# Performance work log

Measured on AMD Instinct MI355X. Metric: run time of the kernel, lower is better.

## Reference

```python
import jax, jax.numpy as jnp
import numpy as np

N, E, IN_FT, OUT_FT = 20000, 4096, 128, 128


def setup_inputs() -> dict:
    key = jax.random.key(0)
    kx, kh, kw = jax.random.split(key, 3)
    X = jax.random.normal(kx, (N, IN_FT), dtype=jnp.float32)
    H = jax.random.randint(kh, (N, E), 0, 2, dtype=jnp.int32)
    weight = jax.random.normal(kw, (IN_FT, OUT_FT), dtype=jnp.float32) * (1.0 / np.sqrt(IN_FT))
    bias = jnp.zeros((OUT_FT,), dtype=jnp.float32)
    return {"X": X, "H": H, "weight": weight, "bias": bias}


def reference(X, H, weight, bias):
    # Dv^{-1/2} H De^{-1} H^T Dv^{-1/2} X W + b, with diag matrices fused as
    # row/column scalings (same math as the torch.diag @ chain, no NxN temporaries).
    Hf = H.astype(jnp.float32)
    v_deg = jnp.sum(Hf, axis=1)            # [N]
    e_deg = jnp.sum(Hf, axis=0)            # [E]
    v_deg = jnp.where(v_deg > 0, v_deg, 1.0)
    e_deg = jnp.where(e_deg > 0, e_deg, 1.0)
    dv_inv_sqrt = 1.0 / jnp.sqrt(v_deg)    # diag(Dv^-1/2)
    de_inv = 1.0 / e_deg                   # diag(De^-1)
    Y = dv_inv_sqrt[:, None] * X
    T = Hf.T @ Y                           # H^T (...)        [E, in]
    T = de_inv[:, None] * T                # De^-1 (...)
    Z = Hf @ T                             # H (...)          [N, in]
    Z = dv_inv_sqrt[:, None] * Z           # Dv^-1/2 (...)
    out = Z @ weight + bias                # [N, out]
    return out
```

## Files before the change

### kernel.cpp

```cpp
#include <hip/hip_runtime.h>

#define NV 20000
#define NE 4096
#define FT 128
#define NW_E 128
#define NW_V 625
#define PT_STRIDE 632
#define NKC 313

typedef __attribute__((ext_vector_type(8))) short short8v;
typedef __attribute__((ext_vector_type(4))) float float4v;

__device__ __forceinline__ unsigned short f2bf(float f) {
    unsigned u = __float_as_uint(f);
    u += 0x7FFFu + ((u >> 16) & 1u);
    return (unsigned short)(u >> 16);
}
__device__ __forceinline__ int lds_off(int r, int chunk) {
    return r * 128 + ((chunk ^ (r & 7)) << 4);
}
__device__ __forceinline__ uint4 lut_entry(int t) {
    uint4 e;
    e.x = ((t & 1) ? 0x3F80u : 0u) | ((t & 2) ? 0x3F800000u : 0u);
    e.y = ((t & 4) ? 0x3F80u : 0u) | ((t & 8) ? 0x3F800000u : 0u);
    e.z = ((t & 16) ? 0x3F80u : 0u) | ((t & 32) ? 0x3F800000u : 0u);
    e.w = ((t & 64) ? 0x3F80u : 0u) | ((t & 128) ? 0x3F800000u : 0u);
    return e;
}

__global__ __launch_bounds__(256) void k_pack(const int* __restrict__ H,
                                              unsigned* __restrict__ packed,
                                              float* __restrict__ dv) {
    __shared__ int cl[4];
    int t = threadIdx.x, wave = t >> 6, lane = t & 63;
    int row = blockIdx.x * 2 + (wave >> 1);
    int half = wave & 1;
    const uint4* base = reinterpret_cast<const uint4*>(H) + (size_t)row * 1024 + half * 512 + lane * 8;
    unsigned m = 0;
#pragma unroll
    for (int i = 0; i < 8; ++i) {
        uint4 v = base[i];
        m |= (v.x ? 1u : 0u) << (i * 4 + 0);
        m |= (v.y ? 1u : 0u) << (i * 4 + 1);
        m |= (v.z ? 1u : 0u) << (i * 4 + 2);
        m |= (v.w ? 1u : 0u) << (i * 4 + 3);
    }
    packed[(size_t)row * NW_E + half * 64 + lane] = m;
    int c = __popc(m);
    for (int o = 32; o > 0; o >>= 1) c += __shfl_down(c, o, 64);
    if (lane == 0) cl[wave] = c;
    __syncthreads();
    if (t < 2) {
        int d = cl[t * 2] + cl[t * 2 + 1];
        dv[blockIdx.x * 2 + t] = d > 0 ? 1.0f / sqrtf((float)d) : 1.0f;
    }
}

__global__ __launch_bounds__(256) void k_btrans(const unsigned* __restrict__ packed,
                                                unsigned* __restrict__ packedT) {
    int lane = threadIdx.x & 63;
    int w = threadIdx.x >> 6;
    int ew = blockIdx.y * 4 + w;
    int n = blockIdx.x * 64 + lane;
    unsigned wv = (n < NV) ? packed[(size_t)n * NW_E + ew] : 0u;
    unsigned my = 0;
#pragma unroll
    for (int j = 0; j < 32; ++j) {
        unsigned long long m = __ballot(((wv >> j) & 1u) != 0);
        unsigned part = (lane < 32) ? (unsigned)m : (unsigned)(m >> 32);
        if ((lane & 31) == j) my = part;
    }
    int nw = blockIdx.x * 2 + (lane >> 5);
    int e = ew * 32 + (lane & 31);
    if (nw <= 625) packedT[(size_t)e * PT_STRIDE + nw] = my;
}

__global__ __launch_bounds__(256) void k_mid(const unsigned* __restrict__ packedT,
                                             const float* __restrict__ X,
                                             const float* __restrict__ dv,
                                             float* __restrict__ de,
                                             unsigned short* __restrict__ At) {
    int b = blockIdx.x, t = threadIdx.x;
    int wave = t >> 6, lane = t & 63;
    if (b < 1024) {
        int e = b * 4 + wave;
        const unsigned* row = packedT + (size_t)e * PT_STRIDE;
        int c = 0;
        for (int i = lane; i < NW_V; i += 64) c += __popc(row[i]);
        for (int o = 32; o > 0; o >>= 1) c += __shfl_down(c, o, 64);
        if (lane == 0) de[e] = c > 0 ? 1.0f / (float)c : 1.0f;
    } else if (b < 2274) {
        int b2 = b - 1024;
        int f = t & 127;
        int nb = (b2 * 2 + (t >> 7)) * 8;
        unsigned short h[8];
#pragma unroll
        for (int i = 0; i < 8; ++i) {
            int n = nb + i;
            h[i] = f2bf(X[(size_t)n * FT + f] * dv[n]);
        }
        uint4 u;
        u.x = (unsigned)h[0] | ((unsigned)h[1] << 16);
        u.y = (unsigned)h[2] | ((unsigned)h[3] << 16);
        u.z = (unsigned)h[4] | ((unsigned)h[5] << 16);
        u.w = (unsigned)h[6] | ((unsigned)h[7] << 16);
        int kc = nb >> 6;
        *reinterpret_cast<uint4*>(At + (size_t)kc * 8192 + f * 64 + (nb & 63)) = u;
    } else {
        int f = t & 127;
        uint4 z = {0, 0, 0, 0};
        *reinterpret_cast<uint4*>(At + (size_t)312 * 8192 + f * 64 + 32 + (t >> 7) * 8) = z;
        *reinterpret_cast<uint4*>(At + (size_t)312 * 8192 + f * 64 + 48 + (t >> 7) * 8) = z;
    }
}

__global__ __launch_bounds__(256, 2) void k_mm1(const unsigned short* __restrict__ At,
                                                const unsigned* __restrict__ packedT,
                                                float* __restrict__ P, int chunkK) {
    __shared__ __align__(16) unsigned char sA[16384];
    __shared__ __align__(16) unsigned char sB[16384];
    __shared__ __align__(16) uint4 slut[256];
    int t = threadIdx.x;
    slut[t] = lut_entry(t);

    int et = blockIdx.x & 31, kp = blockIdx.x >> 5;
    int e0 = et * 128;
    int kbeg = kp * chunkK;
    int kend = kbeg + chunkK; if (kend > NKC * 64) kend = NKC * 64;
    int iters = (kend - kbeg) >> 6; if (iters < 0) iters = 0;

    float4v acc[4][4];
#pragma unroll
    for (int i = 0; i < 4; ++i)
#pragma unroll
        for (int j = 0; j < 4; ++j)
#pragma unroll
            for (int r = 0; r < 4; ++r) acc[i][j][r] = 0.0f;

    int wave = t >> 6, lane = t & 63;
    int wm0 = (wave & 1) * 64, wc0 = (wave >> 1) * 64;
    int r0 = lane & 15, q = lane >> 4;

    const unsigned* brow = packedT + (size_t)(e0 + (t & 127)) * PT_STRIDE + (kbeg >> 5);
    uint4 bw, bw2;
    if (t < 128) bw = *reinterpret_cast<const uint4*>(brow);
    __syncthreads();

    for (int it = 0; it < iters; ++it) {
        int kc = (kbeg >> 6) + it;
        const uint4* slab = reinterpret_cast<const uint4*>(At + (size_t)kc * 8192);
#pragma unroll
        for (int c = 0; c < 4; ++c) {
            int idx = c * 256 + t;
            uint4 v = slab[idx];
            *reinterpret_cast<uint4*>(sA + lds_off(idx >> 3, idx & 7)) = v;
        }
        if (t < 128) {
            unsigned w0, w1;
            if (!(it & 1)) {
                bw2 = *reinterpret_cast<const uint4*>(brow + 2 * it + 4);
                w0 = bw.x; w1 = bw.y;
            } else {
                w0 = bw.z; w1 = bw.w;
            }
            int rB = t;
#pragma unroll
            for (int c = 0; c < 4; ++c)
                *reinterpret_cast<uint4*>(sB + lds_off(rB, c)) = slut[(w0 >> (c * 8)) & 0xFF];
#pragma unroll
            for (int c = 0; c < 4; ++c)
                *reinterpret_cast<uint4*>(sB + lds_off(rB, 4 + c)) = slut[(w1 >> (c * 8)) & 0xFF];
            if (it & 1) bw = bw2;
        }
        __syncthreads();
#pragma unroll
        for (int ks = 0; ks < 2; ++ks) {
            short8v a[4], bb[4];
#pragma unroll
            for (int mi = 0; mi < 4; ++mi)
                a[mi] = *reinterpret_cast<const short8v*>(sA + lds_off(wm0 + mi * 16 + r0, ks * 4 + q));
#pragma unroll
            for (int ci = 0; ci < 4; ++ci)
                bb[ci] = *reinterpret_cast<const short8v*>(sB + lds_off(wc0 + ci * 16 + r0, ks * 4 + q));
#pragma unroll
            for (int mi = 0; mi < 4; ++mi)
#pragma unroll
                for (int ci = 0; ci < 4; ++ci)
                    acc[mi][ci] = __builtin_amdgcn_mfma_f32_16x16x32_bf16(a[mi], bb[ci], acc[mi][ci], 0, 0, 0);
        }
        __syncthreads();
    }
    float* Pp = P + (size_t)kp * (128 * 4096);
#pragma unroll
    for (int mi = 0; mi < 4; ++mi)
#pragma unroll
        for (int ci = 0; ci < 4; ++ci) {
            int f = wm0 + mi * 16 + q * 4;
            int e = e0 + wc0 + ci * 16 + r0;
#pragma unroll
            for (int r = 0; r < 4; ++r)
                Pp[(size_t)(f + r) * 4096 + e] = acc[mi][ci][r];
        }
}

__global__ __launch_bounds__(256) void k_reduce(const float4v* __restrict__ P,
                                                float4v* __restrict__ Tt, int S) {
    int i = blockIdx.x * 256 + threadIdx.x;
    float4v a = P[i];
    for (int p = 1; p < S; ++p) a += P[(size_t)p * 131072 + i];
    Tt[i] = a;
}

__global__ __launch_bounds__(256) void k_ut(const float* __restrict__ Tt,
                                            const float* __restrict__ W,
                                            const float* __restrict__ de,
                                            unsigned short* __restrict__ Ut) {
    int t = threadIdx.x;
    int bx = blockIdx.x;
    int e = bx * 64 + (t & 63);
    int g0 = blockIdx.y * 16 + (t >> 6) * 4;
    float a0 = 0, a1 = 0, a2 = 0, a3 = 0;
    for (int f = 0; f < 128; ++f) {
        float tv = Tt[(size_t)f * 4096 + e];
        float4 wv = *reinterpret_cast<const float4*>(W + f * 128 + g0);
        a0 += tv * wv.x; a1 += tv * wv.y; a2 += tv * wv.z; a3 += tv * wv.w;
    }
    float d = de[e];
    int j = t & 63;
    Ut[(size_t)bx * 8192 + (g0 + 0) * 64 + j] = f2bf(a0 * d);
    Ut[(size_t)bx * 8192 + (g0 + 1) * 64 + j] = f2bf(a1 * d);
    Ut[(size_t)bx * 8192 + (g0 + 2) * 64 + j] = f2bf(a2 * d);
    Ut[(size_t)bx * 8192 + (g0 + 3) * 64 + j] = f2bf(a3 * d);
}

__global__ __launch_bounds__(256, 4) void k_mm2(const unsigned* __restrict__ packed,
                                                const unsigned short* __restrict__ Ut,
                                                const float* __restrict__ dv,
                                                const float* __restrict__ bias,
                                                float* __restrict__ out) {
    __shared__ __align__(16) unsigned char sA[16384];
    __shared__ __align__(16) unsigned char sB[4096];
    __shared__ __align__(16) uint4 slut[256];
    int t = threadIdx.x;
    slut[t] = lut_entry(t);

    int mt = blockIdx.x >> 2, qg = blockIdx.x & 3;
    int n0 = mt * 128, g0 = qg * 32;

    float4v acc[4];
#pragma unroll
    for (int i = 0; i < 4; ++i)
#pragma unroll
        for (int r = 0; r < 4; ++r) acc[i][r] = 0.0f;

    int wave = t >> 6, lane = t & 63;
    int wm0 = (wave & 1) * 64, wc0 = (wave >> 1) * 16;
    int r0 = lane & 15, q = lane >> 4;

    const unsigned* arow = packed + (size_t)(n0 + (t & 127)) * NW_E;
    const unsigned short* bbase = Ut + (size_t)qg * 2048;
    int t2 = t - 128;
    uint4 aw, aw2;
    if (t < 128) aw = *reinterpret_cast<const uint4*>(arow);
    __syncthreads();

    for (int it = 0; it < 64; ++it) {
        if (t < 128) {
            unsigned w0, w1;
            if (!(it & 1)) {
                aw2 = *reinterpret_cast<const uint4*>(arow + 2 * it + 4);
                w0 = aw.x; w1 = aw.y;
            } else {
                w0 = aw.z; w1 = aw.w;
            }
            int rA = t;
#pragma unroll
            for (int c = 0; c < 4; ++c)
                *reinterpret_cast<uint4*>(sA + lds_off(rA, c)) = slut[(w0 >> (c * 8)) & 0xFF];
#pragma unroll
            for (int c = 0; c < 4; ++c)
                *reinterpret_cast<uint4*>(sA + lds_off(rA, 4 + c)) = slut[(w1 >> (c * 8)) & 0xFF];
            if (it & 1) aw = aw2;
        } else {
            const uint4* src = reinterpret_cast<const uint4*>(bbase + (size_t)it * 8192);
#pragma unroll
            for (int c = 0; c < 2; ++c) {
                int idx = t2 * 2 + c;
                uint4 v = src[idx];
                *reinterpret_cast<uint4*>(sB + lds_off(idx >> 3, idx & 7)) = v;
            }
        }
        __syncthreads();
#pragma unroll
        for (int ks = 0; ks < 2; ++ks) {
            short8v a[4], bb;
#pragma unroll
            for (int mi = 0; mi < 4; ++mi)
                a[mi] = *reinterpret_cast<const short8v*>(sA + lds_off(wm0 + mi * 16 + r0, ks * 4 + q));
            bb = *reinterpret_cast<const short8v*>(sB + lds_off(wc0 + r0, ks * 4 + q));
#pragma unroll
            for (int mi = 0; mi < 4; ++mi)
                acc[mi] = __builtin_amdgcn_mfma_f32_16x16x32_bf16(a[mi], bb, acc[mi], 0, 0, 0);
        }
        __syncthreads();
    }
    {
        int g = g0 + wc0 + r0;
        float bg = bias[g];
#pragma unroll
        for (int mi = 0; mi < 4; ++mi) {
#pragma unroll
            for (int r = 0; r < 4; ++r) {
                int n = n0 + wm0 + mi * 16 + q * 4 + r;
                if (n < NV) out[(size_t)n * 128 + g] = dv[n] * acc[mi][r] + bg;
            }
        }
    }
}

extern "C" void kernel_launch(void* const* d_in, const int* in_sizes, int n_in,
                              void* d_out, int out_size, void* d_ws, size_t ws_size,
                              hipStream_t stream) {
    const float* X    = (const float*)d_in[0];
    const int*   H    = (const int*)d_in[1];
    const float* W    = (const float*)d_in[2];
    const float* bias = (const float*)d_in[3];
    float* out = (float*)d_out;

    char* ws = (char*)d_ws;
    size_t off = 0;
    auto alloc = [&](size_t sz) { char* p = ws + off; off += (sz + 255) & ~(size_t)255; return p; };
    unsigned*       packed  = (unsigned*)alloc((size_t)NV * NW_E * 4);
    unsigned*       packedT = (unsigned*)alloc((size_t)NE * PT_STRIDE * 4);
    unsigned short* At      = (unsigned short*)alloc((size_t)NKC * 8192 * 2);
    float*          Tt      = (float*)alloc((size_t)FT * NE * 4);
    unsigned short* Ut      = (unsigned short*)alloc((size_t)FT * NE * 2);
    float*          dv      = (float*)alloc((size_t)NV * 4);
    float*          de      = (float*)alloc((size_t)NE * 4);
    size_t fixed = off;

    long long avail = (long long)ws_size - (long long)fixed;
    int S = (int)(avail / (128LL * 4096 * 4));
    if (S > 16) S = 16;
    if (S < 1) S = 1;
    float* P1 = (float*)(ws + fixed);
    int chunkK = ((NKC * 64 + S * 64 - 1) / (S * 64)) * 64;

    k_pack  <<<NV / 2, 256, 0, stream>>>(H, packed, dv);
    k_btrans<<<dim3(313, 32), 256, 0, stream>>>(packed, packedT);
    k_mid   <<<2275, 256, 0, stream>>>(packedT, X, dv, de, At);
    k_mm1   <<<32 * S, 256, 0, stream>>>(At, packedT, P1, chunkK);
    k_reduce<<<512, 256, 0, stream>>>((const float4v*)P1, (float4v*)Tt, S);
    k_ut    <<<dim3(64, 8), 256, 0, stream>>>(Tt, W, de, Ut);
    k_mm2   <<<628, 256, 0, stream>>>(packed, Ut, dv, bias, out);
}
```

Measured before the change: 592.8 us.

## Double K-tile depth, use direct global-to-LDS loads, fold edge-degree count into transpose

Both bf16 MFMA GEMM kernels now process 128-wide K slabs instead of 64, so the per-iteration barrier and bit-unpack overhead is amortized over twice the MFMA work. The A and B operand tiles are pre-swizzled in global memory so they can be copied straight into LDS with global_load_lds, skipping the register round trip. The edge-degree reduction moves out of k_mid into atomics inside the bit-transpose kernel, removing a separate pass over packedT. LDS usage doubles, which may lower occupancy. k_mm2 launch bounds drop to 3 blocks per SM.

```diff
diff --git a/kernel.cpp b/kernel.cpp
--- a/kernel.cpp
+++ b/kernel.cpp
@@ -6,7 +6,8 @@
 #define NW_E 128
 #define NW_V 625
 #define PT_STRIDE 632
-#define NKC 313
+#define NKC2 157
+#define K_TOT 20096
 
 typedef __attribute__((ext_vector_type(8))) short short8v;
 typedef __attribute__((ext_vector_type(4))) float float4v;
@@ -16,8 +17,8 @@
     u += 0x7FFFu + ((u >> 16) & 1u);
     return (unsigned short)(u >> 16);
 }
-__device__ __forceinline__ int lds_off(int r, int chunk) {
-    return r * 128 + ((chunk ^ (r & 7)) << 4);
+__device__ __forceinline__ int lds_off(int r, int c) {
+    return r * 256 + ((c ^ (r & 15)) << 4);
 }
 __device__ __forceinline__ uint4 lut_entry(int t) {
     uint4 e;
@@ -27,12 +28,18 @@
     e.w = ((t & 64) ? 0x3F80u : 0u) | ((t & 128) ? 0x3F800000u : 0u);
     return e;
 }
+__device__ __forceinline__ void cp16(void* l, const void* g) {
+    __builtin_amdgcn_global_load_lds((__attribute__((address_space(1))) void*)g,
+                                     (__attribute__((address_space(3))) void*)l, 16, 0, 0);
+}
 
 __global__ __launch_bounds__(256) void k_pack(const int* __restrict__ H,
                                               unsigned* __restrict__ packed,
-                                              float* __restrict__ dv) {
+                                              float* __restrict__ dv,
+                                              int* __restrict__ de_cnt) {
     __shared__ int cl[4];
     int t = threadIdx.x, wave = t >> 6, lane = t & 63;
+    if (blockIdx.x < 16) de_cnt[blockIdx.x * 256 + t] = 0;
     int row = blockIdx.x * 2 + (wave >> 1);
     int half = wave & 1;
     const uint4* base = reinterpret_cast<const uint4*>(H) + (size_t)row * 1024 + half * 512 + lane * 8;
@@ -57,7 +64,8 @@
 }
 
 __global__ __launch_bounds__(256) void k_btrans(const unsigned* __restrict__ packed,
-                                                unsigned* __restrict__ packedT) {
+                                                unsigned* __restrict__ packedT,
+                                                int* __restrict__ de_cnt) {
     int lane = threadIdx.x & 63;
     int w = threadIdx.x >> 6;
     int ew = blockIdx.y * 4 + w;
@@ -73,52 +81,40 @@
     int nw = blockIdx.x * 2 + (lane >> 5);
     int e = ew * 32 + (lane & 31);
     if (nw <= 625) packedT[(size_t)e * PT_STRIDE + nw] = my;
-}
-
-__global__ __launch_bounds__(256) void k_mid(const unsigned* __restrict__ packedT,
-                                             const float* __restrict__ X,
+    int cnt = __popc(my);
+    cnt += __shfl_down(cnt, 32, 64);
+    if (lane < 32) atomicAdd(de_cnt + e, cnt);
+}
+
+__global__ __launch_bounds__(256) void k_mid(const float* __restrict__ X,
                                              const float* __restrict__ dv,
-                                             float* __restrict__ de,
                                              unsigned short* __restrict__ At) {
-    int b = blockIdx.x, t = threadIdx.x;
-    int wave = t >> 6, lane = t & 63;
-    if (b < 1024) {
-        int e = b * 4 + wave;
-        const unsigned* row = packedT + (size_t)e * PT_STRIDE;
-        int c = 0;
-        for (int i = lane; i < NW_V; i += 64) c += __popc(row[i]);
-        for (int o = 32; o > 0; o >>= 1) c += __shfl_down(c, o, 64);
-        if (lane == 0) de[e] = c > 0 ? 1.0f / (float)c : 1.0f;
-    } else if (b < 2274) {
-        int b2 = b - 1024;
-        int f = t & 127;
-        int nb = (b2 * 2 + (t >> 7)) * 8;
-        unsigned short h[8];
-#pragma unroll
-        for (int i = 0; i < 8; ++i) {
-            int n = nb + i;
-            h[i] = f2bf(X[(size_t)n * FT + f] * dv[n]);
-        }
-        uint4 u;
-        u.x = (unsigned)h[0] | ((unsigned)h[1] << 16);
-        u.y = (unsigned)h[2] | ((unsigned)h[3] << 16);
-        u.z = (unsigned)h[4] | ((unsigned)h[5] << 16);
-        u.w = (unsigned)h[6] | ((unsigned)h[7] << 16);
-        int kc = nb >> 6;
-        *reinterpret_cast<uint4*>(At + (size_t)kc * 8192 + f * 64 + (nb & 63)) = u;
-    } else {
-        int f = t & 127;
-        uint4 z = {0, 0, 0, 0};
-        *reinterpret_cast<uint4*>(At + (size_t)312 * 8192 + f * 64 + 32 + (t >> 7) * 8) = z;
-        *reinterpret_cast<uint4*>(At + (size_t)312 * 8192 + f * 64 + 48 + (t >> 7) * 8) = z;
-    }
+    int t = threadIdx.x;
+    int f = t & 127;
+    int item = blockIdx.x * 2 + (t >> 7);
+    int nbase = item * 8;
+    unsigned short h[8];
+#pragma unroll
+    for (int i = 0; i < 8; ++i) {
+        int n = nbase + i;
+        float v = (n < NV) ? X[(size_t)n * FT + f] * dv[n] : 0.0f;
+        h[i] = f2bf(v);
+    }
+    uint4 u;
+    u.x = (unsigned)h[0] | ((unsigned)h[1] << 16);
+    u.y = (unsigned)h[2] | ((unsigned)h[3] << 16);
+    u.z = (unsigned)h[4] | ((unsigned)h[5] << 16);
+    u.w = (unsigned)h[6] | ((unsigned)h[7] << 16);
+    int kc2 = nbase >> 7;
+    int c = (nbase >> 3) & 15;
+    *reinterpret_cast<uint4*>(At + (size_t)kc2 * 16384 + f * 128 + ((c ^ (f & 15)) << 3)) = u;
 }
 
 __global__ __launch_bounds__(256, 2) void k_mm1(const unsigned short* __restrict__ At,
                                                 const unsigned* __restrict__ packedT,
                                                 float* __restrict__ P, int chunkK) {
-    __shared__ __align__(16) unsigned char sA[16384];
-    __shared__ __align__(16) unsigned char sB[16384];
+    __shared__ __align__(16) unsigned char sA[32768];
+    __shared__ __align__(16) unsigned char sB[32768];
     __shared__ __align__(16) uint4 slut[256];
     int t = threadIdx.x;
     slut[t] = lut_entry(t);
@@ -126,8 +122,8 @@
     int et = blockIdx.x & 31, kp = blockIdx.x >> 5;
     int e0 = et * 128;
     int kbeg = kp * chunkK;
-    int kend = kbeg + chunkK; if (kend > NKC * 64) kend = NKC * 64;
-    int iters = (kend - kbeg) >> 6; if (iters < 0) iters = 0;
+    int kend = kbeg + chunkK; if (kend > K_TOT) kend = K_TOT;
+    int iters = (kend - kbeg) >> 7; if (iters < 0) iters = 0;
 
     float4v acc[4][4];
 #pragma unroll
@@ -141,40 +137,30 @@
     int wm0 = (wave & 1) * 64, wc0 = (wave >> 1) * 64;
     int r0 = lane & 15, q = lane >> 4;
 
-    const unsigned* brow = packedT + (size_t)(e0 + (t & 127)) * PT_STRIDE + (kbeg >> 5);
-    uint4 bw, bw2;
-    if (t < 128) bw = *reinterpret_cast<const uint4*>(brow);
+    const uint4* brow4 = reinterpret_cast<const uint4*>(
+        packedT + (size_t)(e0 + (t & 127)) * PT_STRIDE + (kbeg >> 5));
+    uint4 bw;
+    if (t < 128 && iters > 0) bw = *brow4;
     __syncthreads();
 
+    const char* gA = reinterpret_cast<const char*>(At) + (size_t)(kbeg >> 7) * 32768 + wave * 8192 + lane * 16;
+    char* lA = reinterpret_cast<char*>(sA) + wave * 8192;
+
     for (int it = 0; it < iters; ++it) {
-        int kc = (kbeg >> 6) + it;
-        const uint4* slab = reinterpret_cast<const uint4*>(At + (size_t)kc * 8192);
-#pragma unroll
-        for (int c = 0; c < 4; ++c) {
-            int idx = c * 256 + t;
-            uint4 v = slab[idx];
-            *reinterpret_cast<uint4*>(sA + lds_off(idx >> 3, idx & 7)) = v;
-        }
+        const char* g = gA + (size_t)it * 32768;
+#pragma unroll
+        for (int j = 0; j < 8; ++j) cp16(lA + j * 1024, g + j * 1024);
         if (t < 128) {
-            unsigned w0, w1;
-            if (!(it & 1)) {
-                bw2 = *reinterpret_cast<const uint4*>(brow + 2 * it + 4);
-                w0 = bw.x; w1 = bw.y;
-            } else {
-                w0 = bw.z; w1 = bw.w;
-            }
-            int rB = t;
-#pragma unroll
-            for (int c = 0; c < 4; ++c)
-                *reinterpret_cast<uint4*>(sB + lds_off(rB, c)) = slut[(w0 >> (c * 8)) & 0xFF];
-#pragma unroll
-            for (int c = 0; c < 4; ++c)
-                *reinterpret_cast<uint4*>(sB + lds_off(rB, 4 + c)) = slut[(w1 >> (c * 8)) & 0xFF];
-            if (it & 1) bw = bw2;
+            uint4 nxt = brow4[it + 1];
+            unsigned wd[4] = {bw.x, bw.y, bw.z, bw.w};
+#pragma unroll
+            for (int c = 0; c < 16; ++c)
+                *reinterpret_cast<uint4*>(sB + lds_off(t, c)) = slut[(wd[c >> 2] >> ((c & 3) * 8)) & 0xFF];
+            bw = nxt;
         }
         __syncthreads();
 #pragma unroll
-        for (int ks = 0; ks < 2; ++ks) {
+        for (int ks = 0; ks < 4; ++ks) {
             short8v a[4], bb[4];
 #pragma unroll
             for (int mi = 0; mi < 4; ++mi)
@@ -213,11 +199,12 @@
 
 __global__ __launch_bounds__(256) void k_ut(const float* __restrict__ Tt,
                                             const float* __restrict__ W,
-                                            const float* __restrict__ de,
+                                            const int* __restrict__ de_cnt,
                                             unsigned short* __restrict__ Ut) {
     int t = threadIdx.x;
     int bx = blockIdx.x;
-    int e = bx * 64 + (t & 63);
+    int j = t & 63;
+    int e = bx * 64 + j;
     int g0 = blockIdx.y * 16 + (t >> 6) * 4;
     float a0 = 0, a1 = 0, a2 = 0, a3 = 0;
     for (int f = 0; f < 128; ++f) {
@@ -225,21 +212,27 @@
         float4 wv = *reinterpret_cast<const float4*>(W + f * 128 + g0);
         a0 += tv * wv.x; a1 += tv * wv.y; a2 += tv * wv.z; a3 += tv * wv.w;
     }
-    float d = de[e];
-    int j = t & 63;
-    Ut[(size_t)bx * 8192 + (g0 + 0) * 64 + j] = f2bf(a0 * d);
-    Ut[(size_t)bx * 8192 + (g0 + 1) * 64 + j] = f2bf(a1 * d);
-    Ut[(size_t)bx * 8192 + (g0 + 2) * 64 + j] = f2bf(a2 * d);
-    Ut[(size_t)bx * 8192 + (g0 + 3) * 64 + j] = f2bf(a3 * d);
-}
-
-__global__ __launch_bounds__(256, 4) void k_mm2(const unsigned* __restrict__ packed,
+    int cnt = de_cnt[e];
+    float d = cnt > 0 ? 1.0f / (float)cnt : 1.0f;
+    float av[4] = {a0, a1, a2, a3};
+    int slabB = bx >> 1;
+    int chi = ((bx & 1) << 3) | (j >> 3);
+    int pos = j & 7;
+#pragma unroll
+    for (int k = 0; k < 4; ++k) {
+        int g = g0 + k;
+        int qg = g >> 5, gr = g & 31;
+        Ut[(size_t)(qg * 32 + slabB) * 4096 + gr * 128 + ((chi ^ (gr & 15)) << 3) + pos] = f2bf(av[k] * d);
+    }
+}
+
+__global__ __launch_bounds__(256, 3) void k_mm2(const unsigned* __restrict__ packed,
                                                 const unsigned short* __restrict__ Ut,
                                                 const float* __restrict__ dv,
                                                 const float* __restrict__ bias,
                                                 float* __restrict__ out) {
-    __shared__ __align__(16) unsigned char sA[16384];
-    __shared__ __align__(16) unsigned char sB[4096];
+    __shared__ __align__(16) unsigned char sA[32768];
+    __shared__ __align__(16) unsigned char sB[8192];
     __shared__ __align__(16) uint4 slut[256];
     int t = threadIdx.x;
     slut[t] = lut_entry(t);
@@ -257,42 +250,31 @@
     int wm0 = (wave & 1) * 64, wc0 = (wave >> 1) * 16;
     int r0 = lane & 15, q = lane >> 4;
 
-    const unsigned* arow = packed + (size_t)(n0 + (t & 127)) * NW_E;
-    const unsigned short* bbase = Ut + (size_t)qg * 2048;
-    int t2 = t - 128;
-    uint4 aw, aw2;
-    if (t < 128) aw = *reinterpret_cast<const uint4*>(arow);
+    const uint4* arow4 = reinterpret_cast<const uint4*>(packed + (size_t)(n0 + (t & 127)) * NW_E);
+    uint4 aw;
+    if (t < 128) aw = *arow4;
     __syncthreads();
 
-    for (int it = 0; it < 64; ++it) {
+    int wb = wave & 1;
+    const char* gB = reinterpret_cast<const char*>(Ut) + (size_t)(qg * 32) * 8192 + wb * 4096 + lane * 16;
+    char* lB = reinterpret_cast<char*>(sB) + wb * 4096;
+
+    for (int it = 0; it < 32; ++it) {
         if (t < 128) {
-            unsigned w0, w1;
-            if (!(it & 1)) {
-                aw2 = *reinterpret_cast<const uint4*>(arow + 2 * it + 4);
-                w0 = aw.x; w1 = aw.y;
-            } else {
-                w0 = aw.z; w1 = aw.w;
-            }
-            int rA = t;
-#pragma unroll
-            for (int c = 0; c < 4; ++c)
-                *reinterpret_cast<uint4*>(sA + lds_off(rA, c)) = slut[(w0 >> (c * 8)) & 0xFF];
-#pragma unroll
-            for (int c = 0; c < 4; ++c)
-                *reinterpret_cast<uint4*>(sA + lds_off(rA, 4 + c)) = slut[(w1 >> (c * 8)) & 0xFF];
-            if (it & 1) aw = aw2;
+            uint4 nxt = arow4[it + 1];
+            unsigned wd[4] = {aw.x, aw.y, aw.z, aw.w};
+#pragma unroll
+            for (int c = 0; c < 16; ++c)
+                *reinterpret_cast<uint4*>(sA + lds_off(t, c)) = slut[(wd[c >> 2] >> ((c & 3) * 8)) & 0xFF];
+            aw = nxt;
         } else {
-            const uint4* src = reinterpret_cast<const uint4*>(bbase + (size_t)it * 8192);
-#pragma unroll
-            for (int c = 0; c < 2; ++c) {
-                int idx = t2 * 2 + c;
-                uint4 v = src[idx];
-                *reinterpret_cast<uint4*>(sB + lds_off(idx >> 3, idx & 7)) = v;
-            }
+            const char* g = gB + (size_t)it * 8192;
+#pragma unroll
+            for (int j = 0; j < 4; ++j) cp16(lB + j * 1024, g + j * 1024);
         }
         __syncthreads();
 #pragma unroll
-        for (int ks = 0; ks < 2; ++ks) {
+        for (int ks = 0; ks < 4; ++ks) {
             short8v a[4], bb;
 #pragma unroll
             for (int mi = 0; mi < 4; ++mi)
@@ -332,11 +314,11 @@
     auto alloc = [&](size_t sz) { char* p = ws + off; off += (sz + 255) & ~(size_t)255; return p; };
     unsigned*       packed  = (unsigned*)alloc((size_t)NV * NW_E * 4);
     unsigned*       packedT = (unsigned*)alloc((size_t)NE * PT_STRIDE * 4);
-    unsigned short* At      = (unsigned short*)alloc((size_t)NKC * 8192 * 2);
+    unsigned short* At      = (unsigned short*)alloc((size_t)NKC2 * 16384 * 2);
     float*          Tt      = (float*)alloc((size_t)FT * NE * 4);
     unsigned short* Ut      = (unsigned short*)alloc((size_t)FT * NE * 2);
     float*          dv      = (float*)alloc((size_t)NV * 4);
-    float*          de      = (float*)alloc((size_t)NE * 4);
+    int*            de_cnt  = (int*)alloc((size_t)NE * 4);
     size_t fixed = off;
 
     long long avail = (long long)ws_size - (long long)fixed;
@@ -344,13 +326,13 @@
     if (S > 16) S = 16;
     if (S < 1) S = 1;
     float* P1 = (float*)(ws + fixed);
-    int chunkK = ((NKC * 64 + S * 64 - 1) / (S * 64)) * 64;
-
-    k_pack  <<<NV / 2, 256, 0, stream>>>(H, packed, dv);
-    k_btrans<<<dim3(313, 32), 256, 0, stream>>>(packed, packedT);
-    k_mid   <<<2275, 256, 0, stream>>>(packedT, X, dv, de, At);
+    int chunkK = ((NKC2 + S - 1) / S) * 128;
+
+    k_pack  <<<NV / 2, 256, 0, stream>>>(H, packed, dv, de_cnt);
+    k_btrans<<<dim3(313, 32), 256, 0, stream>>>(packed, packedT, de_cnt);
+    k_mid   <<<1256, 256, 0, stream>>>(X, dv, At);
     k_mm1   <<<32 * S, 256, 0, stream>>>(At, packedT, P1, chunkK);
     k_reduce<<<512, 256, 0, stream>>>((const float4v*)P1, (float4v*)Tt, S);
-    k_ut    <<<dim3(64, 8), 256, 0, stream>>>(Tt, W, de, Ut);
+    k_ut    <<<dim3(64, 8), 256, 0, stream>>>(Tt, W, de_cnt, Ut);
     k_mm2   <<<628, 256, 0, stream>>>(packed, Ut, dv, bias, out);
 }
```

New measurement: 587.2 us. Within noise of the previous version (-0.9%).
